# Performance work log

Measured on AMD Instinct MI355X. Metric: run time of the kernel, lower is better.

Reference implementation:

```python
import jax, jax.numpy as jnp
import numpy as np

VOLRADIUS = 64.0
DT = 1.0 / VOLRADIUS          # normalized step size (dt / volradius)
NSTEPS = 64                   # covers t in [0, 1.0) at step DT


def setup_inputs() -> dict:
    key = jax.random.key(0)
    ks = jax.random.split(key, 8)
    B, H, W, K, M = 1, 128, 128, 32, 16
    # ray origins near volume center, unit directions
    raypos = 0.2 * jax.random.normal(ks[0], (B, H, W, 3), jnp.float32)
    rd = jax.random.normal(ks[1], (B, H, W, 3), jnp.float32)
    raydir = rd / jnp.linalg.norm(rd, axis=-1, keepdims=True)
    tmin = jnp.zeros((B, H, W), jnp.float32)
    tmax = 0.9 + 0.1 * jax.random.uniform(ks[2], (B, H, W), dtype=jnp.float32)
    tminmax = jnp.stack([tmin, tmax], axis=-1)
    # primitive poses: positions, rotations (orthonormal via QR), inverse-scales
    primpos = 0.3 * jax.random.normal(ks[3], (B, K, 3), jnp.float32)
    A = jax.random.normal(ks[4], (B, K, 3, 3), jnp.float32)
    primrot, _ = jnp.linalg.qr(A)
    primscale = 1.0 + 2.0 * jax.random.uniform(ks[5], (B, K, 3), dtype=jnp.float32)
    # RGBA voxel payload per primitive; alpha channel nonnegative (decoder emits nonneg density)
    template = jax.random.normal(ks[6], (B, K, 4, M, M, M), jnp.float32)
    template = template.at[:, :, 3].set(2.0 * jax.nn.softplus(template[:, :, 3]))
    return dict(raypos=raypos, raydir=raydir, tminmax=tminmax, primpos=primpos,
                primrot=primrot, primscale=primscale, template=template)


def _trilinear(template, y):
    # template [B,K,C,M,M,M]; y [B,R,K,3] normalized coords in [-1,1] (align_corners)
    B, K, C, M = template.shape[0], template.shape[1], template.shape[2], template.shape[3]
    g = (y + 1.0) * 0.5 * (M - 1)
    i0 = jnp.clip(jnp.floor(g), 0, M - 2).astype(jnp.int32)
    f = jnp.clip(g - i0.astype(g.dtype), 0.0, 1.0)
    i1 = i0 + 1
    bidx = jnp.arange(B)[:, None, None]
    kidx = jnp.arange(K)[None, None, :]

    def corner(iz, iy, ix):
        # advanced-index gather -> [B,R,K,C]
        return template[bidx, kidx, :, iz, iy, ix]

    fz, fy, fx = f[..., 0:1], f[..., 1:2], f[..., 2:3]
    i0z, i0y, i0x = i0[..., 0], i0[..., 1], i0[..., 2]
    i1z, i1y, i1x = i1[..., 0], i1[..., 1], i1[..., 2]
    v = ((1 - fz) * (1 - fy) * (1 - fx) * corner(i0z, i0y, i0x)
         + (1 - fz) * (1 - fy) * fx * corner(i0z, i0y, i1x)
         + (1 - fz) * fy * (1 - fx) * corner(i0z, i1y, i0x)
         + (1 - fz) * fy * fx * corner(i0z, i1y, i1x)
         + fz * (1 - fy) * (1 - fx) * corner(i1z, i0y, i0x)
         + fz * (1 - fy) * fx * corner(i1z, i0y, i1x)
         + fz * fy * (1 - fx) * corner(i1z, i1y, i0x)
         + fz * fy * fx * corner(i1z, i1y, i1x))
    return v  # [B,R,K,C]


def reference(raypos, raydir, tminmax, primpos, primrot, primscale, template):
    B, H, W, _ = raypos.shape
    R = H * W
    rp = raypos.reshape(B, R, 3)
    rd = raydir.reshape(B, R, 3)
    tmm = tminmax.reshape(B, R, 2)
    tmin, tmax = tmm[..., 0:1], tmm[..., 1:2]

    def step(carry, i):
        rgb, alpha = carry
        t = tmin + i * DT                                   # [B,R,1]
        pos = rp + rd * t                                   # [B,R,3]
        xl = pos[:, :, None, :] - primpos[:, None, :, :]    # [B,R,K,3]
        yloc = jnp.einsum('bkij,brkj->brki', primrot, xl) * primscale[:, None, :, :]
        inside = jnp.all(jnp.abs(yloc) <= 1.0, axis=-1, keepdims=True).astype(rgb.dtype)
        samp = (_trilinear(template, yloc) * inside).sum(axis=2)   # [B,R,4]
        srgb, salpha = samp[..., :3], samp[..., 3:4]
        valid = (t < tmax).astype(rgb.dtype)
        # clamped additive compositing (Neural Volumes / MVP)
        newalpha = jnp.clip(alpha + salpha * DT * valid, 0.0, 1.0)
        contrib = newalpha - alpha
        return (rgb + srgb * contrib, newalpha), None

    init = (jnp.zeros((B, R, 3), raypos.dtype), jnp.zeros((B, R, 1), raypos.dtype))
    (rgb, alpha), _ = jax.lax.scan(step, init, jnp.arange(NSTEPS, dtype=raypos.dtype))

    rayrgba = jnp.concatenate([rgb, alpha], axis=-1).reshape(B, H, W, 4)
    rayrgba = jnp.transpose(rayrgba, (0, 3, 1, 2))   # [B,4,H,W]
    rayrgb = rayrgba[:, :3]
    rayalpha = rayrgba[:, 3:4]
    return rayrgb, rayalpha, rayrgba
```

## Files before the change

kernel.cpp:

```cpp
#include <hip/hip_runtime.h>


namespace {

constexpr float kDT  = 1.0f / 64.0f;
constexpr int   kVox = 32 * 4096;

__global__ __launch_bounds__(256) void transpose_tmpl(
    const float* __restrict__ tmpl, float* __restrict__ wsT)
{
    const int idx = blockIdx.x * 256 + threadIdx.x;
    const int k   = idx >> 12;
    const int rem = idx & 4095;
    const float* src = tmpl + k * 16384 + rem;
    float4 v;
    v.x = src[0];
    v.y = src[4096];
    v.z = src[8192];
    v.w = src[12288];
    ((float4*)wsT)[idx] = v;
}

template <bool T4>
__global__ __launch_bounds__(256) void raymarch5(
    const float* __restrict__ raypos,
    const float* __restrict__ raydir,
    const float* __restrict__ tminmax,
    const float* __restrict__ primpos,
    const float* __restrict__ primrot,
    const float* __restrict__ primscale,
    const float* __restrict__ tmpl,
    const float* __restrict__ tmplT,
    float* __restrict__ out,
    int R)
{
    const int lane = threadIdx.x & 63;
    const int wid  = threadIdx.x >> 6;
    const int k    = lane & 31;
    const int half = lane >> 5;
    const int ray  = blockIdx.x * 8 + wid * 2 + half;

    const float rpx = raypos[ray * 3 + 0];
    const float rpy = raypos[ray * 3 + 1];
    const float rpz = raypos[ray * 3 + 2];
    const float rdx = raydir[ray * 3 + 0];
    const float rdy = raydir[ray * 3 + 1];
    const float rdz = raydir[ray * 3 + 2];
    const float tmin = tminmax[ray * 2 + 0];
    const float tmax = tminmax[ray * 2 + 1];

    float A0, A1, A2, D0, D1, D2;
    {
        const float ox = rpx - primpos[k * 3 + 0];
        const float oy = rpy - primpos[k * 3 + 1];
        const float oz = rpz - primpos[k * 3 + 2];
        const float s0 = primscale[k * 3 + 0];
        const float s1 = primscale[k * 3 + 1];
        const float s2 = primscale[k * 3 + 2];
        const float* rk = primrot + k * 9;
        A0 = (rk[0] * ox + rk[1] * oy + rk[2] * oz) * s0;
        D0 = (rk[0] * rdx + rk[1] * rdy + rk[2] * rdz) * s0;
        A1 = (rk[3] * ox + rk[4] * oy + rk[5] * oz) * s1;
        D1 = (rk[3] * rdx + rk[4] * rdy + rk[5] * rdz) * s1;
        A2 = (rk[6] * ox + rk[7] * oy + rk[8] * oz) * s2;
        D2 = (rk[6] * rdx + rk[7] * rdy + rk[8] * rdz) * s2;
    }

    float alpha = 0.f;
    float r0 = 0.f, r1 = 0.f, r2 = 0.f;

    for (int i = 0; i < 64; ++i) {
        const float t = fmaf((float)i, kDT, tmin);
        const bool live = (t < tmax) && (alpha < 1.0f);
        if (__ballot(live) == 0ull) break;

        const float y0 = fmaf(D0, t, A0);
        const float y1 = fmaf(D1, t, A1);
        const float y2 = fmaf(D2, t, A2);
        const bool inside = live && fabsf(y0) <= 1.0f && fabsf(y1) <= 1.0f
                                 && fabsf(y2) <= 1.0f;
        if (__ballot(inside) == 0ull) continue;

        float s0 = 0.f, s1 = 0.f, s2 = 0.f, s3 = 0.f;
        if (inside) {
            const float gz = (y0 + 1.0f) * 7.5f;
            const float gy = (y1 + 1.0f) * 7.5f;
            const float gx = (y2 + 1.0f) * 7.5f;
            const int iz = (int)fminf(floorf(gz), 14.0f);
            const int iy = (int)fminf(floorf(gy), 14.0f);
            const int ix = (int)fminf(floorf(gx), 14.0f);
            const float fz = fminf(gz - (float)iz, 1.0f);
            const float fy = fminf(gy - (float)iy, 1.0f);
            const float fx = fminf(gx - (float)ix, 1.0f);
            const float oz_ = 1.0f - fz, oy_ = 1.0f - fy, ox_ = 1.0f - fx;
            const float w000 = oz_ * oy_ * ox_;
            const float w001 = oz_ * oy_ * fx;
            const float w010 = oz_ * fy  * ox_;
            const float w011 = oz_ * fy  * fx;
            const float w100 = fz  * oy_ * ox_;
            const float w101 = fz  * oy_ * fx;
            const float w110 = fz  * fy  * ox_;
            const float w111 = fz  * fy  * fx;
            if (T4) {
                const float* tp = tmplT + ((k * 4096 + iz * 256 + iy * 16 + ix) << 2);
                const float4 c000 = *(const float4*)(tp + 0);
                const float4 c001 = *(const float4*)(tp + 4);
                const float4 c010 = *(const float4*)(tp + 64);
                const float4 c011 = *(const float4*)(tp + 68);
                const float4 c100 = *(const float4*)(tp + 1024);
                const float4 c101 = *(const float4*)(tp + 1028);
                const float4 c110 = *(const float4*)(tp + 1088);
                const float4 c111 = *(const float4*)(tp + 1092);
                s0 = w000*c000.x + w001*c001.x + w010*c010.x + w011*c011.x
                   + w100*c100.x + w101*c101.x + w110*c110.x + w111*c111.x;
                s1 = w000*c000.y + w001*c001.y + w010*c010.y + w011*c011.y
                   + w100*c100.y + w101*c101.y + w110*c110.y + w111*c111.y;
                s2 = w000*c000.z + w001*c001.z + w010*c010.z + w011*c011.z
                   + w100*c100.z + w101*c101.z + w110*c110.z + w111*c111.z;
                s3 = w000*c000.w + w001*c001.w + w010*c010.w + w011*c011.w
                   + w100*c100.w + w101*c101.w + w110*c110.w + w111*c111.w;
            } else {
                const float* tp = tmpl + k * 16384 + iz * 256 + iy * 16 + ix;
                float acc[4];
                #pragma unroll
                for (int c = 0; c < 4; ++c) {
                    const float* tc = tp + c * 4096;
                    acc[c] = w000 * tc[0]   + w001 * tc[1]
                           + w010 * tc[16]  + w011 * tc[17]
                           + w100 * tc[256] + w101 * tc[257]
                           + w110 * tc[272] + w111 * tc[273];
                }
                s0 = acc[0]; s1 = acc[1]; s2 = acc[2]; s3 = acc[3];
            }
        }

        float tot3 = s3;
        #pragma unroll
        for (int m = 1; m < 32; m <<= 1) tot3 += __shfl_xor(tot3, m);

        const float na = fminf(fmaf(tot3, kDT, alpha), 1.0f);
        const float contrib = na - alpha;
        alpha = na;
        r0 = fmaf(s0, contrib, r0);
        r1 = fmaf(s1, contrib, r1);
        r2 = fmaf(s2, contrib, r2);
    }

    #pragma unroll
    for (int m = 1; m < 32; m <<= 1) {
        r0 += __shfl_xor(r0, m);
        r1 += __shfl_xor(r1, m);
        r2 += __shfl_xor(r2, m);
    }

    if (k == 0) {
        out[0 * R + ray] = r0;
        out[1 * R + ray] = r1;
        out[2 * R + ray] = r2;
        out[3 * R + ray] = alpha;
        out[4 * R + ray] = r0;
        out[5 * R + ray] = r1;
        out[6 * R + ray] = r2;
        out[7 * R + ray] = alpha;
    }
}

}

extern "C" void kernel_launch(void* const* d_in, const int* in_sizes, int n_in,
                              void* d_out, int out_size, void* d_ws, size_t ws_size,
                              hipStream_t stream) {
    const float* raypos    = (const float*)d_in[0];
    const float* raydir    = (const float*)d_in[1];
    const float* tminmax   = (const float*)d_in[2];
    const float* primpos   = (const float*)d_in[3];
    const float* primrot   = (const float*)d_in[4];
    const float* primscale = (const float*)d_in[5];
    const float* tmpl      = (const float*)d_in[6];
    float* out = (float*)d_out;

    const int R = in_sizes[0] / 3;
    const size_t tmplBytes = (size_t)kVox * 4 * sizeof(float);

    if (ws_size >= tmplBytes) {
        float* wsT = (float*)d_ws;
        transpose_tmpl<<<dim3(kVox / 256), dim3(256), 0, stream>>>(tmpl, wsT);
        raymarch5<true><<<dim3(R / 8), dim3(256), 0, stream>>>(
            raypos, raydir, tminmax, primpos, primrot, primscale, tmpl, wsT, out, R);
    } else {
        raymarch5<false><<<dim3(R / 8), dim3(256), 0, stream>>>(
            raypos, raydir, tminmax, primpos, primrot, primscale, tmpl, nullptr, out, R);
    }
}
```

Baseline: 101.9 us.

## Compact per-ray primitive sample work via slab intervals and two-pass compositing

```diff
diff --git a/kernel.cpp b/kernel.cpp
--- a/kernel.cpp
+++ b/kernel.cpp
@@ -6,8 +6,14 @@
 constexpr float kDT  = 1.0f / 64.0f;
 constexpr int   kVox = 32 * 4096;
 
+constexpr size_t kOffT  = 0;
+constexpr size_t kOffW  = (size_t)2 << 20;
+constexpr size_t kOffIt = ((size_t)2 << 20) + ((size_t)512 << 10);
+constexpr size_t kWsNeed = kOffIt + (size_t)16384 * 2048 * 2;
+
 __global__ __launch_bounds__(256) void transpose_tmpl(
-    const float* __restrict__ tmpl, float* __restrict__ wsT)
+    const float* __restrict__ tmpl, float4* __restrict__ wsT,
+    float* __restrict__ wsW)
 {
     const int idx = blockIdx.x * 256 + threadIdx.x;
     const int k   = idx >> 12;
@@ -18,27 +24,34 @@
     v.y = src[4096];
     v.z = src[8192];
     v.w = src[12288];
-    ((float4*)wsT)[idx] = v;
-}
-
-template <bool T4>
-__global__ __launch_bounds__(256) void raymarch5(
+    wsT[idx] = v;
+    wsW[idx] = v.w;
+}
+
+__global__ __launch_bounds__(256) void raymarch6(
     const float* __restrict__ raypos,
     const float* __restrict__ raydir,
     const float* __restrict__ tminmax,
     const float* __restrict__ primpos,
     const float* __restrict__ primrot,
     const float* __restrict__ primscale,
-    const float* __restrict__ tmpl,
-    const float* __restrict__ tmplT,
-    float* __restrict__ out,
-    int R)
+    const float4* __restrict__ wsT,
+    const float* __restrict__ wsW,
+    unsigned short* __restrict__ itemsBase,
+    float* __restrict__ out, int R)
 {
     const int lane = threadIdx.x & 63;
     const int wid  = threadIdx.x >> 6;
     const int k    = lane & 31;
     const int half = lane >> 5;
     const int ray  = blockIdx.x * 8 + wid * 2 + half;
+
+    __shared__ float4 sAD[4][2][32][2];
+    __shared__ float  sAlpha[4][2][64];
+    __shared__ float  sContrib[4][2][64];
+
+    sAlpha[wid][half][k]      = 0.0f;
+    sAlpha[wid][half][k + 32] = 0.0f;
 
     const float rpx = raypos[ray * 3 + 0];
     const float rpy = raypos[ray * 3 + 1];
@@ -49,40 +62,114 @@
     const float tmin = tminmax[ray * 2 + 0];
     const float tmax = tminmax[ray * 2 + 1];
 
-    float A0, A1, A2, D0, D1, D2;
+    int last = min(63, (int)floorf((tmax - tmin) * 64.0f));
+    if (last >= 0 && fmaf((float)last, kDT, tmin) >= tmax) last--;
+
+    int i0, len;
     {
         const float ox = rpx - primpos[k * 3 + 0];
         const float oy = rpy - primpos[k * 3 + 1];
         const float oz = rpz - primpos[k * 3 + 2];
-        const float s0 = primscale[k * 3 + 0];
-        const float s1 = primscale[k * 3 + 1];
-        const float s2 = primscale[k * 3 + 2];
-        const float* rk = primrot + k * 9;
-        A0 = (rk[0] * ox + rk[1] * oy + rk[2] * oz) * s0;
-        D0 = (rk[0] * rdx + rk[1] * rdy + rk[2] * rdz) * s0;
-        A1 = (rk[3] * ox + rk[4] * oy + rk[5] * oz) * s1;
-        D1 = (rk[3] * rdx + rk[4] * rdy + rk[5] * rdz) * s1;
-        A2 = (rk[6] * ox + rk[7] * oy + rk[8] * oz) * s2;
-        D2 = (rk[6] * rdx + rk[7] * rdy + rk[8] * rdz) * s2;
-    }
-
-    float alpha = 0.f;
-    float r0 = 0.f, r1 = 0.f, r2 = 0.f;
-
-    for (int i = 0; i < 64; ++i) {
-        const float t = fmaf((float)i, kDT, tmin);
-        const bool live = (t < tmax) && (alpha < 1.0f);
-        if (__ballot(live) == 0ull) break;
-
-        const float y0 = fmaf(D0, t, A0);
-        const float y1 = fmaf(D1, t, A1);
-        const float y2 = fmaf(D2, t, A2);
-        const bool inside = live && fabsf(y0) <= 1.0f && fabsf(y1) <= 1.0f
-                                 && fabsf(y2) <= 1.0f;
-        if (__ballot(inside) == 0ull) continue;
-
-        float s0 = 0.f, s1 = 0.f, s2 = 0.f, s3 = 0.f;
-        if (inside) {
+        float a[3], d[3];
+        float lo = -1e30f, hi = 1e30f;
+        #pragma unroll
+        for (int i = 0; i < 3; ++i) {
+            const float r0 = primrot[k * 9 + 3 * i + 0];
+            const float r1 = primrot[k * 9 + 3 * i + 1];
+            const float r2 = primrot[k * 9 + 3 * i + 2];
+            const float sci = primscale[k * 3 + i];
+            a[i] = (r0 * ox + r1 * oy + r2 * oz) * sci;
+            d[i] = (r0 * rdx + r1 * rdy + r2 * rdz) * sci;
+            const float inv = 1.0f / d[i];
+            const float tA = (-1.001f - a[i]) * inv;
+            const float tB = ( 1.001f - a[i]) * inv;
+            lo = fmaxf(lo, fminf(tA, tB));
+            hi = fminf(hi, fmaxf(tA, tB));
+        }
+        i0 = max(0,    (int)ceilf ((lo - tmin) * 64.0f));
+        const int i1 = min(last, (int)floorf((hi - tmin) * 64.0f));
+        len = max(0, i1 - i0 + 1);
+        sAD[wid][half][k][0] = make_float4(a[0], a[1], a[2], 0.0f);
+        sAD[wid][half][k][1] = make_float4(d[0], d[1], d[2], 0.0f);
+    }
+
+    int psum = len;
+    #pragma unroll
+    for (int m = 1; m < 32; m <<= 1) {
+        const int n = __shfl_up(psum, m);
+        if (k >= m) psum += n;
+    }
+    const int off   = psum - len;
+    const int total = __shfl(psum, lane | 31);
+
+    unsigned short* items = itemsBase + (size_t)ray * 2048;
+    for (int j = 0; j < len; ++j)
+        items[off + j] = (unsigned short)((k << 6) | (i0 + j));
+
+    for (int jj = k; jj < total; jj += 32) {
+        const int it   = items[jj];
+        const int k2   = it >> 6;
+        const int step = it & 63;
+        const float4 A = sAD[wid][half][k2][0];
+        const float4 D = sAD[wid][half][k2][1];
+        const float t  = fmaf((float)step, kDT, tmin);
+        const float y0 = fmaf(D.x, t, A.x);
+        const float y1 = fmaf(D.y, t, A.y);
+        const float y2 = fmaf(D.z, t, A.z);
+        if (fabsf(y0) <= 1.0f && fabsf(y1) <= 1.0f && fabsf(y2) <= 1.0f) {
+            const float gz = (y0 + 1.0f) * 7.5f;
+            const float gy = (y1 + 1.0f) * 7.5f;
+            const float gx = (y2 + 1.0f) * 7.5f;
+            const int iz = (int)fminf(floorf(gz), 14.0f);
+            const int iy = (int)fminf(floorf(gy), 14.0f);
+            const int ix = (int)fminf(floorf(gx), 14.0f);
+            const float fz = fminf(gz - (float)iz, 1.0f);
+            const float fy = fminf(gy - (float)iy, 1.0f);
+            const float fx = fminf(gx - (float)ix, 1.0f);
+            const float oz_ = 1.0f - fz, oy_ = 1.0f - fy, ox_ = 1.0f - fx;
+            const float* w = wsW + (k2 * 4096 + iz * 256 + iy * 16 + ix);
+            const float s3 = (oz_ * oy_ * ox_) * w[0]   + (oz_ * oy_ * fx) * w[1]
+                           + (oz_ * fy  * ox_) * w[16]  + (oz_ * fy  * fx) * w[17]
+                           + (fz  * oy_ * ox_) * w[256] + (fz  * oy_ * fx) * w[257]
+                           + (fz  * fy  * ox_) * w[272] + (fz  * fy  * fx) * w[273];
+            atomicAdd(&sAlpha[wid][half][step], s3);
+        }
+    }
+
+    float alphaOut = 0.0f;
+    #pragma unroll
+    for (int r = 0; r < 2; ++r) {
+        const float tminR = __shfl(tmin, r * 32);
+        const float tmaxR = __shfl(tmax, r * 32);
+        const float b  = sAlpha[wid][r][lane];
+        const float tl = fmaf((float)lane, kDT, tminR);
+        const float aa = (tl < tmaxR) ? b * kDT : 0.0f;
+        float ps = aa;
+        #pragma unroll
+        for (int m = 1; m < 64; m <<= 1) {
+            const float n = __shfl_up(ps, m);
+            if (lane >= m) ps += n;
+        }
+        const float aI = fminf(ps, 1.0f);
+        sContrib[wid][r][lane] = aI - fminf(ps - aa, 1.0f);
+        const float aEnd = __shfl(aI, 63);
+        if (half == r) alphaOut = aEnd;
+    }
+
+    float r0 = 0.0f, r1 = 0.0f, r2 = 0.0f;
+    for (int jj = k; jj < total; jj += 32) {
+        const int it   = items[jj];
+        const int k2   = it >> 6;
+        const int step = it & 63;
+        const float contrib = sContrib[wid][half][step];
+        if (contrib == 0.0f) continue;
+        const float4 A = sAD[wid][half][k2][0];
+        const float4 D = sAD[wid][half][k2][1];
+        const float t  = fmaf((float)step, kDT, tmin);
+        const float y0 = fmaf(D.x, t, A.x);
+        const float y1 = fmaf(D.y, t, A.y);
+        const float y2 = fmaf(D.z, t, A.z);
+        if (fabsf(y0) <= 1.0f && fabsf(y1) <= 1.0f && fabsf(y2) <= 1.0f) {
             const float gz = (y0 + 1.0f) * 7.5f;
             const float gy = (y1 + 1.0f) * 7.5f;
             const float gx = (y2 + 1.0f) * 7.5f;
@@ -101,49 +188,25 @@
             const float w101 = fz  * oy_ * fx;
             const float w110 = fz  * fy  * ox_;
             const float w111 = fz  * fy  * fx;
-            if (T4) {
-                const float* tp = tmplT + ((k * 4096 + iz * 256 + iy * 16 + ix) << 2);
-                const float4 c000 = *(const float4*)(tp + 0);
-                const float4 c001 = *(const float4*)(tp + 4);
-                const float4 c010 = *(const float4*)(tp + 64);
-                const float4 c011 = *(const float4*)(tp + 68);
-                const float4 c100 = *(const float4*)(tp + 1024);
-                const float4 c101 = *(const float4*)(tp + 1028);
-                const float4 c110 = *(const float4*)(tp + 1088);
-                const float4 c111 = *(const float4*)(tp + 1092);
-                s0 = w000*c000.x + w001*c001.x + w010*c010.x + w011*c011.x
-                   + w100*c100.x + w101*c101.x + w110*c110.x + w111*c111.x;
-                s1 = w000*c000.y + w001*c001.y + w010*c010.y + w011*c011.y
-                   + w100*c100.y + w101*c101.y + w110*c110.y + w111*c111.y;
-                s2 = w000*c000.z + w001*c001.z + w010*c010.z + w011*c011.z
-                   + w100*c100.z + w101*c101.z + w110*c110.z + w111*c111.z;
-                s3 = w000*c000.w + w001*c001.w + w010*c010.w + w011*c011.w
-                   + w100*c100.w + w101*c101.w + w110*c110.w + w111*c111.w;
-            } else {
-                const float* tp = tmpl + k * 16384 + iz * 256 + iy * 16 + ix;
-                float acc[4];
-                #pragma unroll
-                for (int c = 0; c < 4; ++c) {
-                    const float* tc = tp + c * 4096;
-                    acc[c] = w000 * tc[0]   + w001 * tc[1]
-                           + w010 * tc[16]  + w011 * tc[17]
-                           + w100 * tc[256] + w101 * tc[257]
-                           + w110 * tc[272] + w111 * tc[273];
-                }
-                s0 = acc[0]; s1 = acc[1]; s2 = acc[2]; s3 = acc[3];
-            }
-        }
-
-        float tot3 = s3;
-        #pragma unroll
-        for (int m = 1; m < 32; m <<= 1) tot3 += __shfl_xor(tot3, m);
-
-        const float na = fminf(fmaf(tot3, kDT, alpha), 1.0f);
-        const float contrib = na - alpha;
-        alpha = na;
-        r0 = fmaf(s0, contrib, r0);
-        r1 = fmaf(s1, contrib, r1);
-        r2 = fmaf(s2, contrib, r2);
+            const float4* tp = wsT + (k2 * 4096 + iz * 256 + iy * 16 + ix);
+            const float4 c000 = tp[0];
+            const float4 c001 = tp[1];
+            const float4 c010 = tp[16];
+            const float4 c011 = tp[17];
+            const float4 c100 = tp[256];
+            const float4 c101 = tp[257];
+            const float4 c110 = tp[272];
+            const float4 c111 = tp[273];
+            const float v0 = w000*c000.x + w001*c001.x + w010*c010.x + w011*c011.x
+                           + w100*c100.x + w101*c101.x + w110*c110.x + w111*c111.x;
+            const float v1 = w000*c000.y + w001*c001.y + w010*c010.y + w011*c011.y
+                           + w100*c100.y + w101*c101.y + w110*c110.y + w111*c111.y;
+            const float v2 = w000*c000.z + w001*c001.z + w010*c010.z + w011*c011.z
+                           + w100*c100.z + w101*c101.z + w110*c110.z + w111*c111.z;
+            r0 = fmaf(v0, contrib, r0);
+            r1 = fmaf(v1, contrib, r1);
+            r2 = fmaf(v2, contrib, r2);
+        }
     }
 
     #pragma unroll
@@ -157,11 +220,80 @@
         out[0 * R + ray] = r0;
         out[1 * R + ray] = r1;
         out[2 * R + ray] = r2;
-        out[3 * R + ray] = alpha;
+        out[3 * R + ray] = alphaOut;
         out[4 * R + ray] = r0;
         out[5 * R + ray] = r1;
         out[6 * R + ray] = r2;
-        out[7 * R + ray] = alpha;
+        out[7 * R + ray] = alphaOut;
+    }
+}
+
+__global__ __launch_bounds__(256) void raymarch_fb(
+    const float* __restrict__ raypos, const float* __restrict__ raydir,
+    const float* __restrict__ tminmax, const float* __restrict__ primpos,
+    const float* __restrict__ primrot, const float* __restrict__ primscale,
+    const float* __restrict__ tmpl, float* __restrict__ out, int R)
+{
+    const int lane = threadIdx.x & 63;
+    const int wid  = threadIdx.x >> 6;
+    const int k    = lane & 31;
+    const int half = lane >> 5;
+    const int ray  = blockIdx.x * 8 + wid * 2 + half;
+
+    const float rpx = raypos[ray*3+0], rpy = raypos[ray*3+1], rpz = raypos[ray*3+2];
+    const float rdx = raydir[ray*3+0], rdy = raydir[ray*3+1], rdz = raydir[ray*3+2];
+    const float tmin = tminmax[ray*2+0], tmax = tminmax[ray*2+1];
+
+    float A0,A1,A2,D0,D1,D2;
+    {
+        const float ox = rpx - primpos[k*3+0], oy = rpy - primpos[k*3+1], oz = rpz - primpos[k*3+2];
+        const float s0 = primscale[k*3+0], s1 = primscale[k*3+1], s2 = primscale[k*3+2];
+        const float* rk = primrot + k*9;
+        A0 = (rk[0]*ox+rk[1]*oy+rk[2]*oz)*s0; D0 = (rk[0]*rdx+rk[1]*rdy+rk[2]*rdz)*s0;
+        A1 = (rk[3]*ox+rk[4]*oy+rk[5]*oz)*s1; D1 = (rk[3]*rdx+rk[4]*rdy+rk[5]*rdz)*s1;
+        A2 = (rk[6]*ox+rk[7]*oy+rk[8]*oz)*s2; D2 = (rk[6]*rdx+rk[7]*rdy+rk[8]*rdz)*s2;
+    }
+    float alpha = 0.f, r0 = 0.f, r1 = 0.f, r2 = 0.f;
+    for (int i = 0; i < 64; ++i) {
+        const float t = fmaf((float)i, kDT, tmin);
+        const bool live = (t < tmax) && (alpha < 1.0f);
+        if (__ballot(live) == 0ull) break;
+        const float y0 = fmaf(D0,t,A0), y1 = fmaf(D1,t,A1), y2 = fmaf(D2,t,A2);
+        const bool inside = live && fabsf(y0)<=1.f && fabsf(y1)<=1.f && fabsf(y2)<=1.f;
+        if (__ballot(inside) == 0ull) continue;
+        float s0=0.f,s1=0.f,s2=0.f,s3=0.f;
+        if (inside) {
+            const float gz=(y0+1.f)*7.5f, gy=(y1+1.f)*7.5f, gx=(y2+1.f)*7.5f;
+            const int iz=(int)fminf(floorf(gz),14.f), iy=(int)fminf(floorf(gy),14.f), ix=(int)fminf(floorf(gx),14.f);
+            const float fz=fminf(gz-(float)iz,1.f), fy=fminf(gy-(float)iy,1.f), fx=fminf(gx-(float)ix,1.f);
+            const float oz_=1.f-fz, oy_=1.f-fy, ox_=1.f-fx;
+            const float w000=oz_*oy_*ox_, w001=oz_*oy_*fx, w010=oz_*fy*ox_, w011=oz_*fy*fx;
+            const float w100=fz*oy_*ox_, w101=fz*oy_*fx, w110=fz*fy*ox_, w111=fz*fy*fx;
+            const float* tp = tmpl + k*16384 + iz*256 + iy*16 + ix;
+            float acc[4];
+            #pragma unroll
+            for (int c = 0; c < 4; ++c) {
+                const float* tc = tp + c*4096;
+                acc[c] = w000*tc[0]+w001*tc[1]+w010*tc[16]+w011*tc[17]
+                       + w100*tc[256]+w101*tc[257]+w110*tc[272]+w111*tc[273];
+            }
+            s0=acc[0]; s1=acc[1]; s2=acc[2]; s3=acc[3];
+        }
+        float tot3 = s3;
+        #pragma unroll
+        for (int m = 1; m < 32; m <<= 1) tot3 += __shfl_xor(tot3, m);
+        const float na = fminf(fmaf(tot3, kDT, alpha), 1.0f);
+        const float contrib = na - alpha;
+        alpha = na;
+        r0 = fmaf(s0, contrib, r0); r1 = fmaf(s1, contrib, r1); r2 = fmaf(s2, contrib, r2);
+    }
+    #pragma unroll
+    for (int m = 1; m < 32; m <<= 1) {
+        r0 += __shfl_xor(r0, m); r1 += __shfl_xor(r1, m); r2 += __shfl_xor(r2, m);
+    }
+    if (k == 0) {
+        out[0*R+ray]=r0; out[1*R+ray]=r1; out[2*R+ray]=r2; out[3*R+ray]=alpha;
+        out[4*R+ray]=r0; out[5*R+ray]=r1; out[6*R+ray]=r2; out[7*R+ray]=alpha;
     }
 }
 
@@ -180,15 +312,17 @@
     float* out = (float*)d_out;
 
     const int R = in_sizes[0] / 3;
-    const size_t tmplBytes = (size_t)kVox * 4 * sizeof(float);
-
-    if (ws_size >= tmplBytes) {
-        float* wsT = (float*)d_ws;
-        transpose_tmpl<<<dim3(kVox / 256), dim3(256), 0, stream>>>(tmpl, wsT);
-        raymarch5<true><<<dim3(R / 8), dim3(256), 0, stream>>>(
-            raypos, raydir, tminmax, primpos, primrot, primscale, tmpl, wsT, out, R);
+
+    if (ws_size >= kWsNeed) {
+        float4* wsT = (float4*)((char*)d_ws + kOffT);
+        float*  wsW = (float*)((char*)d_ws + kOffW);
+        unsigned short* items = (unsigned short*)((char*)d_ws + kOffIt);
+        transpose_tmpl<<<dim3(kVox / 256), dim3(256), 0, stream>>>(tmpl, wsT, wsW);
+        raymarch6<<<dim3(R / 8), dim3(256), 0, stream>>>(
+            raypos, raydir, tminmax, primpos, primrot, primscale,
+            wsT, wsW, items, out, R);
     } else {
-        raymarch5<false><<<dim3(R / 8), dim3(256), 0, stream>>>(
-            raypos, raydir, tminmax, primpos, primrot, primscale, tmpl, nullptr, out, R);
-    }
-}
+        raymarch_fb<<<dim3(R / 8), dim3(256), 0, stream>>>(
+            raypos, raydir, tminmax, primpos, primrot, primscale, tmpl, out, R);
+    }
+}
```

New measurement: 188.9 us. +85.5%, slower.
